# Optimization experiments

Hardware: AMD Instinct MI355X
Metric: run time of the kernel (lower is better)

The kernel has to match this reference:

```python
import math
import jax, jax.numpy as jnp
import numpy as np

B, NQ, NK, DIM, H, HD = 2, 1024, 2048, 1024, 16, 64


def setup_inputs() -> dict:
    key = jax.random.key(0)
    ks = jax.random.split(key, 12)
    s = 1.0 / math.sqrt(DIM)
    return {
        "q": jax.random.normal(ks[0], (B, NQ, DIM), jnp.float32),
        "k": jax.random.normal(ks[1], (B, NK, DIM), jnp.float32),
        "v": jax.random.normal(ks[2], (B, NK, DIM), jnp.float32),
        "distances": jax.random.uniform(ks[3], (B, NQ, NK), jnp.float32),
        "attn_mask": jax.random.bernoulli(ks[4], 0.5, (B, NQ, NK)),
        "key_padding_mask_q": jax.random.bernoulli(ks[5], 0.5, (B, NQ)),
        "key_padding_mask_k": jax.random.bernoulli(ks[6], 0.5, (B, NK)),
        "Wq": jax.random.normal(ks[7], (H * HD, DIM), jnp.float32) * s,
        "Wk": jax.random.normal(ks[8], (H * HD, DIM), jnp.float32) * s,
        "Wv": jax.random.normal(ks[9], (H * HD, DIM), jnp.float32) * s,
        "Wo": jax.random.normal(ks[10], (DIM, H * HD), jnp.float32) * s,
        "gate_alpha": jnp.float32(0.1),
    }


def reference(q, k, v, distances, attn_mask, key_padding_mask_q,
              key_padding_mask_k, Wq, Wk, Wv, Wo, gate_alpha):
    bsz, q_len, _ = q.shape
    k_len = k.shape[1]
    neg = jnp.finfo(q.dtype).min

    # projections -> (B, H, N, HD)
    qp = (q @ Wq.T).reshape(bsz, q_len, H, HD).transpose(0, 2, 1, 3)
    kp = (k @ Wk.T).reshape(bsz, k_len, H, HD).transpose(0, 2, 1, 3)
    vp = (v @ Wv.T).reshape(bsz, k_len, H, HD).transpose(0, 2, 1, 3)

    scores = jnp.einsum('bhqd,bhkd->bhqk', qp, kp) / math.sqrt(HD)
    scores = jnp.where(attn_mask[:, None, :, :], scores, neg)
    scores = jnp.where(key_padding_mask_k[:, None, None, :], scores, neg)

    attn = jax.nn.softmax(scores, axis=-1)  # (B,H,NQ,NK)

    # distance gating: mask, batch-mean normalize, exponential gate
    d = distances * attn_mask.astype(distances.dtype)
    d = d * key_padding_mask_k[:, None, :].astype(d.dtype)
    mean = d.sum(axis=(-1, -2)) / (q_len * k_len + 1e-6)
    mean = jnp.maximum(mean, 1e-6)[:, None, None]
    d = d / mean
    alpha = jax.nn.softplus(gate_alpha)
    gate = jnp.exp(-alpha * d)[:, None, :, :]  # (B,1,NQ,NK)

    w = attn * gate
    w = w / (w.sum(axis=-1, keepdims=True) + 1e-6)

    out = jnp.einsum('bhqk,bhkd->bhqd', w, vp)
    out = out.transpose(0, 2, 1, 3).reshape(bsz, q_len, H * HD)
    out = out * key_padding_mask_q[:, :, None].astype(out.dtype)
    return out @ Wo.T
```

## Files before the change

kernel.cpp:

```cpp
#include <hip/hip_runtime.h>
#include <hip/hip_bf16.h>
#include <cfloat>

#define B_   2
#define NQ_  1024
#define NK_  2048
#define H_   16
#define HD_  64
#define VPAD 2176
#define GPAD 2112

typedef float  floatx4 __attribute__((ext_vector_type(4)));
typedef __bf16 bf16x8  __attribute__((ext_vector_type(8)));
typedef __bf16 bf16x4  __attribute__((ext_vector_type(4)));

static __device__ __forceinline__ floatx4 mfma16(bf16x8 a, bf16x8 b, floatx4 c) {
    return __builtin_amdgcn_mfma_f32_16x16x32_bf16(a, b, c, 0, 0, 0);
}

static __device__ __forceinline__ void gl_lds(const __bf16* g, __bf16* lbase,
                                              int lane) {
#if __has_builtin(__builtin_amdgcn_global_load_lds)
    __builtin_amdgcn_global_load_lds(
        (const __attribute__((address_space(1))) void*)g,
        (__attribute__((address_space(3))) void*)lbase, 16, 0, 0);
#else
    *(bf16x8*)(lbase + lane * 8) = *(const bf16x8*)g;
#endif
}

struct CvtArgs {
    const float* src[7];
    __bf16*      dst[7];
};

__global__ __launch_bounds__(256) void cvt_mean_kernel(
    CvtArgs a, const float* __restrict__ dist, const int* __restrict__ amask,
    const int* __restrict__ kpmk, float* __restrict__ msum,
    __bf16* __restrict__ dmask)
{
    if (blockIdx.x >= 1792) {
        const int mb = blockIdx.x - 1792;
        const int b  = mb >> 9;
        const float* d  = dist  + (size_t)b * NQ_ * NK_;
        const int*   am = amask + (size_t)b * NQ_ * NK_;
        const int*   km = kpmk  + b * NK_;
        __bf16*      dm = dmask + (size_t)b * NQ_ * GPAD;
        const int base = (mb & 511) * 256 + threadIdx.x;
        float s = 0.f;
        #pragma unroll
        for (int j = 0; j < 4; j++) {
            const int i   = base + j * 131072;
            const int idx = i * 4;
            const int kk  = idx & (NK_ - 1);
            const int q   = i >> 9;
            float4 dv = *(const float4*)(d + idx);
            int4   mv = *(const int4*)(am + idx);
            int4   kv = *(const int4*)(km + kk);
            bf16x4 o;
            if (mv.x && kv.x) { s += dv.x; o[0] = (__bf16)dv.x; } else o[0] = (__bf16)3e38f;
            if (mv.y && kv.y) { s += dv.y; o[1] = (__bf16)dv.y; } else o[1] = (__bf16)3e38f;
            if (mv.z && kv.z) { s += dv.z; o[2] = (__bf16)dv.z; } else o[2] = (__bf16)3e38f;
            if (mv.w && kv.w) { s += dv.w; o[3] = (__bf16)dv.w; } else o[3] = (__bf16)3e38f;
            *(bf16x4*)&dm[(size_t)q * GPAD + kk] = o;
        }
        #pragma unroll
        for (int off = 32; off >= 1; off >>= 1) s += __shfl_down(s, off);
        __shared__ float wsum[4];
        if ((threadIdx.x & 63) == 0) wsum[threadIdx.x >> 6] = s;
        __syncthreads();
        if (threadIdx.x == 0)
            atomicAdd(&msum[b], wsum[0] + wsum[1] + wsum[2] + wsum[3]);
        return;
    }
    #pragma unroll
    for (int j = 0; j < 4; j++) {
        size_t r = (size_t)blockIdx.x * 1024 + j * 256 + threadIdx.x;
        int s;
        if (r < 262144)                  { s = 0; }
        else if ((r -= 262144) < 524288) { s = 1; }
        else if ((r -= 524288) < 524288) { s = 2; }
        else { r -= 524288; s = 3 + (int)(r >> 17); r &= 131071; }
        const float* sp = a.src[s] + r * 8;
        float4 f0 = *(const float4*)sp;
        float4 f1 = *(const float4*)(sp + 4);
        bf16x8 o;
        o[0] = (__bf16)f0.x; o[1] = (__bf16)f0.y; o[2] = (__bf16)f0.z; o[3] = (__bf16)f0.w;
        o[4] = (__bf16)f1.x; o[5] = (__bf16)f1.y; o[6] = (__bf16)f1.z; o[7] = (__bf16)f1.w;
        *(bf16x8*)(a.dst[s] + r * 8) = o;
    }
}

template <typename EPI>
static __device__ __forceinline__ void gemm128_core(
    const __bf16* __restrict__ A, const __bf16* __restrict__ Bw,
    int m0, int n0, __bf16* As, __bf16* Bs, EPI epi)
{
    const int t    = threadIdx.x;
    const int w    = t >> 6, lane = t & 63;
    const int lrow = lane & 15, quad = lane >> 4;
    const int lr   = lane >> 2, lc = lane & 3;

    floatx4 acc[4][4];
    #pragma unroll
    for (int mi = 0; mi < 4; mi++)
        #pragma unroll
        for (int ni = 0; ni < 4; ni++) acc[mi][ni] = floatx4{0.f, 0.f, 0.f, 0.f};

    const __bf16* ga = A  + (size_t)(m0 + w * 32 + lr) * 1024 + lc * 8;
    const __bf16* gb = Bw + (size_t)(n0 + w * 32 + lr) * 1024 + lc * 8;

    for (int k0 = 0; k0 < 1024; k0 += 64) {
        __syncthreads();
        #pragma unroll
        for (int h = 0; h < 2; h++) {
            gl_lds(ga + k0 + h * 32,             &As[h * 4096 + (w * 32) * 32],      lane);
            gl_lds(ga + k0 + h * 32 + 16 * 1024, &As[h * 4096 + (w * 32 + 16) * 32], lane);
            gl_lds(gb + k0 + h * 32,             &Bs[h * 4096 + (w * 32) * 32],      lane);
            gl_lds(gb + k0 + h * 32 + 16 * 1024, &Bs[h * 4096 + (w * 32 + 16) * 32], lane);
        }
        __syncthreads();

        #pragma unroll
        for (int h = 0; h < 2; h++) {
            bf16x8 af[4], bfr[4];
            #pragma unroll
            for (int mi = 0; mi < 4; mi++)
                af[mi] = *(const bf16x8*)
                    &As[h * 4096 + ((w & 1) * 64 + mi * 16 + lrow) * 32 + quad * 8];
            #pragma unroll
            for (int ni = 0; ni < 4; ni++)
                bfr[ni] = *(const bf16x8*)
                    &Bs[h * 4096 + ((w >> 1) * 64 + ni * 16 + lrow) * 32 + quad * 8];
            #pragma unroll
            for (int mi = 0; mi < 4; mi++)
                #pragma unroll
                for (int ni = 0; ni < 4; ni++)
                    acc[mi][ni] = mfma16(af[mi], bfr[ni], acc[mi][ni]);
        }
    }

    #pragma unroll
    for (int mi = 0; mi < 4; mi++)
        #pragma unroll
        for (int ni = 0; ni < 4; ni++)
            #pragma unroll
            for (int r = 0; r < 4; r++) {
                const int m = m0 + (w & 1) * 64 + mi * 16 + quad * 4 + r;
                const int n = n0 + (w >> 1) * 64 + ni * 16 + lrow;
                epi(m, n, acc[mi][ni][r]);
            }
}

template <typename EPI>
static __device__ __forceinline__ void gemm64_core(
    const __bf16* __restrict__ A, const __bf16* __restrict__ Bw,
    int m0, int n0, EPI epi)
{
    __shared__ alignas(16) __bf16 As[2][64 * 32];
    __shared__ alignas(16) __bf16 Bs[2][128 * 32];
    const int t    = threadIdx.x;
    const int w    = t >> 6, lane = t & 63;
    const int lrow = lane & 15, quad = lane >> 4;
    const int lr   = lane >> 2, lc = lane & 3;

    floatx4 acc[4][2];
    #pragma unroll
    for (int mi = 0; mi < 4; mi++)
        #pragma unroll
        for (int ni = 0; ni < 2; ni++) acc[mi][ni] = floatx4{0.f, 0.f, 0.f, 0.f};

    const __bf16* ga = A  + (size_t)(m0 + w * 16 + lr) * 1024 + lc * 8;
    const __bf16* gb = Bw + (size_t)(n0 + w * 32 + lr) * 1024 + lc * 8;

    for (int k0 = 0; k0 < 1024; k0 += 64) {
        __syncthreads();
        #pragma unroll
        for (int h = 0; h < 2; h++) {
            gl_lds(ga + k0 + h * 32,             &As[h][(w * 16) * 32],      lane);
            gl_lds(gb + k0 + h * 32,             &Bs[h][(w * 32) * 32],      lane);
            gl_lds(gb + k0 + h * 32 + 16 * 1024, &Bs[h][(w * 32 + 16) * 32], lane);
        }
        __syncthreads();

        #pragma unroll
        for (int h = 0; h < 2; h++) {
            bf16x8 af[4], bfr[2];
            #pragma unroll
            for (int mi = 0; mi < 4; mi++)
                af[mi] = *(const bf16x8*)
                    &As[h][(mi * 16 + lrow) * 32 + quad * 8];
            #pragma unroll
            for (int ni = 0; ni < 2; ni++)
                bfr[ni] = *(const bf16x8*)
                    &Bs[h][(w * 32 + ni * 16 + lrow) * 32 + quad * 8];
            #pragma unroll
            for (int mi = 0; mi < 4; mi++)
                #pragma unroll
                for (int ni = 0; ni < 2; ni++)
                    acc[mi][ni] = mfma16(af[mi], bfr[ni], acc[mi][ni]);
        }
    }

    #pragma unroll
    for (int mi = 0; mi < 4; mi++)
        #pragma unroll
        for (int ni = 0; ni < 2; ni++)
            #pragma unroll
            for (int r = 0; r < 4; r++) {
                const int m = m0 + mi * 16 + quad * 4 + r;
                const int n = n0 + w * 32 + ni * 16 + lrow;
                epi(m, n, acc[mi][ni][r]);
            }
}

__global__ __launch_bounds__(256) void proj_kernel(
    const __bf16* __restrict__ qb, const __bf16* __restrict__ kb,
    const __bf16* __restrict__ vb, const __bf16* __restrict__ wqb,
    const __bf16* __restrict__ wkb, const __bf16* __restrict__ wvb,
    __bf16* __restrict__ qp, __bf16* __restrict__ kp,
    __bf16* __restrict__ vpT)
{
    __shared__ alignas(16) __bf16 As[2 * 128 * 32];
    __shared__ alignas(16) __bf16 Bs[2 * 128 * 32];
    const int z = blockIdx.z;
    if (z == 0) {
        if ((int)blockIdx.x >= 16) return;
        gemm128_core(qb, wqb, blockIdx.x * 128, blockIdx.y * 128, As, Bs,
                     [&](int m, int n, float v) {
            const int b = m >> 10, q = m & 1023;
            const int h = n >> 6,  d = n & 63;
            qp[(((size_t)(b * 16 + h) * NQ_ + q) << 6) + d] = (__bf16)v;
        });
    } else if (z == 1) {
        gemm128_core(kb, wkb, blockIdx.x * 128, blockIdx.y * 128, As, Bs,
                     [&](int m, int n, float v) {
            const int b = m >> 11, key = m & 2047;
            const int h = n >> 6,  d = n & 63;
            kp[(((size_t)(b * 16 + h) * NK_ + key) << 6) + d] = (__bf16)v;
        });
    } else {
        gemm128_core(wvb, vb, blockIdx.y * 128, blockIdx.x * 128, As, Bs,
                     [&](int m, int n, float v) {
            const int h = m >> 6,  d = m & 63;
            const int b = n >> 11, key = n & 2047;
            vpT[((size_t)(b * 16 + h) * HD_ + d) * VPAD + key] = (__bf16)v;
        });
    }
}

__global__ __launch_bounds__(256) void oproj_kernel(
    const __bf16* __restrict__ A, const __bf16* __restrict__ W,
    float* __restrict__ Cout)
{
    const int m0 = blockIdx.x * 64, n0 = blockIdx.y * 128;
    gemm64_core(A, W, m0, n0, [&](int m, int n, float v) {
        Cout[(size_t)m * 1024 + n] = v;
    });
}

__global__ __launch_bounds__(256, 2) void attn_kernel(
    const __bf16* __restrict__ qp, const __bf16* __restrict__ kp,
    const __bf16* __restrict__ vpT, const __bf16* __restrict__ dmask,
    const float* __restrict__ msum, const float* __restrict__ galpha,
    const int* __restrict__ kpmq, __bf16* __restrict__ attnout)
{
    __shared__ __bf16 Ks[64 * 72];
    __shared__ __bf16 Vt[2][64 * 72];
    __shared__ __bf16 Ps[4][2][16 * 72];
    const int t    = threadIdx.x;
    const int w    = t >> 6, lane = t & 63;
    const int lrow = lane & 15, quad = lane >> 4;
    const int qt   = blockIdx.x;
    const int bh   = blockIdx.y;
    const int b    = bh >> 4, h = bh & 15;
    const int q0   = qt * 64 + w * 16;
    const int NT   = NK_ / 64;

    const float mean  = fmaxf(msum[b] / ((float)(NQ_ * NK_) + 1e-6f), 1e-6f);
    const float alpha = log1pf(__expf(galpha[0]));
    const float cg    = -alpha / mean;

    const __bf16* qb = qp + ((size_t)bh * NQ_ + q0 + lrow) * HD_ + quad * 8;
    const bf16x8 qf0 = *(const bf16x8*)qb;
    const bf16x8 qf1 = *(const bf16x8*)(qb + 32);

    const int srow0 = t >> 3,        sc0 = t & 7;
    const int srow1 = 32 + (t >> 3), sc1 = t & 7;
    const int so0 = srow0 * 72 + sc0 * 8;
    const int so1 = srow1 * 72 + sc1 * 8;
    const __bf16* Kg = kp  + (size_t)bh * NK_ * HD_;
    const __bf16* Vg = vpT + (size_t)bh * HD_ * VPAD;
    const __bf16* grow = dmask + ((size_t)b * NQ_ + q0 + lrow) * GPAD;

    float G = 0.f;
    floatx4 O[4];
    #pragma unroll
    for (int nb = 0; nb < 4; nb++) O[nb] = floatx4{0.f, 0.f, 0.f, 0.f};

    bf16x8 kr0, kr1, vr0, vr1;
    bf16x4 gr[4];
    auto loadt = [&](int kb) {
        kr0 = *(const bf16x8*)(Kg + (size_t)(kb + srow0) * HD_ + sc0 * 8);
        kr1 = *(const bf16x8*)(Kg + (size_t)(kb + srow1) * HD_ + sc1 * 8);
        vr0 = *(const bf16x8*)(Vg + (size_t)srow0 * VPAD + kb + sc0 * 8);
        vr1 = *(const bf16x8*)(Vg + (size_t)srow1 * VPAD + kb + sc1 * 8);
        #pragma unroll
        for (int c = 0; c < 4; c++)
            gr[c] = *(const bf16x4*)(grow + kb + c * 16 + quad * 4);
    };
    loadt(0);

    for (int ib = 0; ib < NT; ib++) {
        const int kb  = ib * 64;
        const int cur = ib & 1;

        __syncthreads();
        *(bf16x8*)&Ks[so0]      = kr0;
        *(bf16x8*)&Ks[so1]      = kr1;
        *(bf16x8*)&Vt[cur][so0] = vr0;
        *(bf16x8*)&Vt[cur][so1] = vr1;
        __syncthreads();

        bf16x4 gcur[4];
        #pragma unroll
        for (int c = 0; c < 4; c++) gcur[c] = gr[c];
        if (ib + 1 < NT) loadt(kb + 64);

        floatx4 s4[4];
        #pragma unroll
        for (int c = 0; c < 4; c++) {
            bf16x8 kf0 = *(const bf16x8*)&Ks[(c * 16 + lrow) * 72 + quad * 8];
            bf16x8 kf1 = *(const bf16x8*)&Ks[(c * 16 + lrow) * 72 + 32 + quad * 8];
            floatx4 a = floatx4{0.f, 0.f, 0.f, 0.f};
            a = mfma16(kf0, qf0, a);
            a = mfma16(kf1, qf1, a);
            s4[c] = a;
        }

        if (ib > 0) {
            const int prv = cur ^ 1;
            bf16x8 pf0 = *(const bf16x8*)&Ps[w][prv][lrow * 72 + quad * 8];
            bf16x8 pf1 = *(const bf16x8*)&Ps[w][prv][lrow * 72 + 32 + quad * 8];
            #pragma unroll
            for (int nb = 0; nb < 4; nb++) {
                bf16x8 vf0 = *(const bf16x8*)
                    &Vt[prv][(nb * 16 + lrow) * 72 + quad * 8];
                bf16x8 vf1 = *(const bf16x8*)
                    &Vt[prv][(nb * 16 + lrow) * 72 + 32 + quad * 8];
                O[nb] = mfma16(pf0, vf0, O[nb]);
                O[nb] = mfma16(pf1, vf1, O[nb]);
            }
        }

        #pragma unroll
        for (int c = 0; c < 4; c++) {
            const float e0 = __expf(fmaf(s4[c][0], 0.125f, cg * (float)gcur[c][0]));
            const float e1 = __expf(fmaf(s4[c][1], 0.125f, cg * (float)gcur[c][1]));
            const float e2 = __expf(fmaf(s4[c][2], 0.125f, cg * (float)gcur[c][2]));
            const float e3 = __expf(fmaf(s4[c][3], 0.125f, cg * (float)gcur[c][3]));
            G += (e0 + e1) + (e2 + e3);
            bf16x4 pk;
            pk[0] = (__bf16)e0; pk[1] = (__bf16)e1;
            pk[2] = (__bf16)e2; pk[3] = (__bf16)e3;
            *(bf16x4*)&Ps[w][cur][lrow * 72 + c * 16 + quad * 4] = pk;
        }
    }

    {
        const int prv = (NT - 1) & 1;
        bf16x8 pf0 = *(const bf16x8*)&Ps[w][prv][lrow * 72 + quad * 8];
        bf16x8 pf1 = *(const bf16x8*)&Ps[w][prv][lrow * 72 + 32 + quad * 8];
        #pragma unroll
        for (int nb = 0; nb < 4; nb++) {
            bf16x8 vf0 = *(const bf16x8*)&Vt[prv][(nb * 16 + lrow) * 72 + quad * 8];
            bf16x8 vf1 = *(const bf16x8*)&Vt[prv][(nb * 16 + lrow) * 72 + 32 + quad * 8];
            O[nb] = mfma16(pf0, vf0, O[nb]);
            O[nb] = mfma16(pf1, vf1, O[nb]);
        }
    }

    G += __shfl_xor(G, 16);
    G += __shfl_xor(G, 32);

    #pragma unroll
    for (int r = 0; r < 4; r++) {
        const int q  = q0 + quad * 4 + r;
        const float gq = __shfl(G, quad * 4 + r);
        const float f  = kpmq[b * NQ_ + q] ? 1.f / (gq + 1e-30f) : 0.f;
        #pragma unroll
        for (int nb = 0; nb < 4; nb++) {
            attnout[((size_t)b * NQ_ + q) * 1024 + h * HD_ + nb * 16 + lrow] =
                (__bf16)(O[nb][r] * f);
        }
    }
}

extern "C" void kernel_launch(void* const* d_in, const int* in_sizes, int n_in,
                              void* d_out, int out_size, void* d_ws,
                              size_t ws_size, hipStream_t stream)
{
    const float* q      = (const float*)d_in[0];
    const float* k      = (const float*)d_in[1];
    const float* v      = (const float*)d_in[2];
    const float* dist   = (const float*)d_in[3];
    const int*   amask  = (const int*)d_in[4];
    const int*   kpmq   = (const int*)d_in[5];
    const int*   kpmk   = (const int*)d_in[6];
    const float* Wq     = (const float*)d_in[7];
    const float* Wk     = (const float*)d_in[8];
    const float* Wv     = (const float*)d_in[9];
    const float* Wo     = (const float*)d_in[10];
    const float* galpha = (const float*)d_in[11];

    char* p = (char*)d_ws;
    float*  msum = (float*)p;                 p += 256;
    __bf16* qb   = (__bf16*)p;                p += (size_t)2097152 * 2;
    __bf16* kb   = (__bf16*)p;                p += (size_t)4194304 * 2;
    __bf16* vb   = (__bf16*)p;                p += (size_t)4194304 * 2;
    __bf16* wqb  = (__bf16*)p;                p += (size_t)1048576 * 2;
    __bf16* wkb  = (__bf16*)p;                p += (size_t)1048576 * 2;
    __bf16* wvb  = (__bf16*)p;                p += (size_t)1048576 * 2;
    __bf16* wob  = (__bf16*)p;                p += (size_t)1048576 * 2;
    __bf16* qp   = (__bf16*)p;                p += (size_t)2097152 * 2;
    __bf16* kpb  = (__bf16*)p;                p += (size_t)4194304 * 2;
    __bf16* vpT  = (__bf16*)p;                p += (size_t)32 * 64 * VPAD * 2;
    __bf16* dmask = (__bf16*)p;               p += (size_t)2048 * GPAD * 2;
    __bf16* attnout = (__bf16*)p;             p += (size_t)2097152 * 2;

    CvtArgs ca;
    ca.src[0] = q;  ca.src[1] = k;  ca.src[2] = v;
    ca.src[3] = Wq; ca.src[4] = Wk; ca.src[5] = Wv; ca.src[6] = Wo;
    ca.dst[0] = qb;  ca.dst[1] = kb;  ca.dst[2] = vb;
    ca.dst[3] = wqb; ca.dst[4] = wkb; ca.dst[5] = wvb; ca.dst[6] = wob;

    hipMemsetAsync(msum, 0, 256, stream);
    cvt_mean_kernel<<<2816, 256, 0, stream>>>(ca, dist, amask, kpmk, msum,
                                              dmask);
    proj_kernel<<<dim3(32, 8, 3), 256, 0, stream>>>(qb, kb, vb, wqb, wkb, wvb,
                                                    qp, kpb, vpT);
    attn_kernel<<<dim3(16, 32), 256, 0, stream>>>(qp, kpb, vpT, dmask,
                                                  msum, galpha, kpmq, attnout);
    oproj_kernel<<<dim3(32, 8), 256, 0, stream>>>(attnout, wob, (float*)d_out);
}
```

Baseline: 245.6 us.

## Split key range across two wave groups per block and merge partials in LDS

The attention kernel now runs 512 threads per block, with two groups of four waves each processing half of the key sequence for the same query tile. Partial output accumulators and row sums from the second group are written to shared memory and added by the first group before normalization. This doubles the number of waves in flight and halves each wave's serial loop. In exchange it drops the one-tile-delayed PV pipelining, adds LDS usage and a final merge step with extra barriers.

Measured after the change: 248.2 us. About the same (+1.0%).

```diff
diff --git a/kernel.cpp b/kernel.cpp
--- a/kernel.cpp
+++ b/kernel.cpp
@@ -259,23 +259,28 @@
     });
 }
 
-__global__ __launch_bounds__(256, 2) void attn_kernel(
+__global__ __launch_bounds__(512, 4) void attn_kernel(
     const __bf16* __restrict__ qp, const __bf16* __restrict__ kp,
     const __bf16* __restrict__ vpT, const __bf16* __restrict__ dmask,
     const float* __restrict__ msum, const float* __restrict__ galpha,
     const int* __restrict__ kpmq, __bf16* __restrict__ attnout)
 {
-    __shared__ __bf16 Ks[64 * 72];
+    __shared__ __bf16 Ks[2][64 * 72];
     __shared__ __bf16 Vt[2][64 * 72];
-    __shared__ __bf16 Ps[4][2][16 * 72];
+    __shared__ __bf16 Ps[8][16 * 72];
+    __shared__ float  Ox[4][16][68];
+    __shared__ float  Gx[4][16];
     const int t    = threadIdx.x;
     const int w    = t >> 6, lane = t & 63;
+    const int g    = w >> 2;
+    const int wg   = w & 3;
     const int lrow = lane & 15, quad = lane >> 4;
     const int qt   = blockIdx.x;
     const int bh   = blockIdx.y;
     const int b    = bh >> 4, h = bh & 15;
-    const int q0   = qt * 64 + w * 16;
-    const int NT   = NK_ / 64;
+    const int q0   = qt * 64 + wg * 16;
+    const int k0   = g * (NK_ / 2);
+    const int NT   = (NK_ / 2) / 64;
 
     const float mean  = fmaxf(msum[b] / ((float)(NQ_ * NK_) + 1e-6f), 1e-6f);
     const float alpha = log1pf(__expf(galpha[0]));
@@ -285,8 +290,9 @@
     const bf16x8 qf0 = *(const bf16x8*)qb;
     const bf16x8 qf1 = *(const bf16x8*)(qb + 32);
 
-    const int srow0 = t >> 3,        sc0 = t & 7;
-    const int srow1 = 32 + (t >> 3), sc1 = t & 7;
+    const int tg    = t & 255;
+    const int srow0 = tg >> 3,        sc0 = tg & 7;
+    const int srow1 = 32 + (tg >> 3), sc1 = tg & 7;
     const int so0 = srow0 * 72 + sc0 * 8;
     const int so1 = srow1 * 72 + sc1 * 8;
     const __bf16* Kg = kp  + (size_t)bh * NK_ * HD_;
@@ -309,17 +315,16 @@
         for (int c = 0; c < 4; c++)
             gr[c] = *(const bf16x4*)(grow + kb + c * 16 + quad * 4);
     };
-    loadt(0);
+    loadt(k0);
 
     for (int ib = 0; ib < NT; ib++) {
-        const int kb  = ib * 64;
-        const int cur = ib & 1;
-
-        __syncthreads();
-        *(bf16x8*)&Ks[so0]      = kr0;
-        *(bf16x8*)&Ks[so1]      = kr1;
-        *(bf16x8*)&Vt[cur][so0] = vr0;
-        *(bf16x8*)&Vt[cur][so1] = vr1;
+        const int kb = k0 + ib * 64;
+
+        __syncthreads();
+        *(bf16x8*)&Ks[g][so0] = kr0;
+        *(bf16x8*)&Ks[g][so1] = kr1;
+        *(bf16x8*)&Vt[g][so0] = vr0;
+        *(bf16x8*)&Vt[g][so1] = vr1;
         __syncthreads();
 
         bf16x4 gcur[4];
@@ -330,27 +335,12 @@
         floatx4 s4[4];
         #pragma unroll
         for (int c = 0; c < 4; c++) {
-            bf16x8 kf0 = *(const bf16x8*)&Ks[(c * 16 + lrow) * 72 + quad * 8];
-            bf16x8 kf1 = *(const bf16x8*)&Ks[(c * 16 + lrow) * 72 + 32 + quad * 8];
+            bf16x8 kf0 = *(const bf16x8*)&Ks[g][(c * 16 + lrow) * 72 + quad * 8];
+            bf16x8 kf1 = *(const bf16x8*)&Ks[g][(c * 16 + lrow) * 72 + 32 + quad * 8];
             floatx4 a = floatx4{0.f, 0.f, 0.f, 0.f};
             a = mfma16(kf0, qf0, a);
             a = mfma16(kf1, qf1, a);
             s4[c] = a;
-        }
-
-        if (ib > 0) {
-            const int prv = cur ^ 1;
-            bf16x8 pf0 = *(const bf16x8*)&Ps[w][prv][lrow * 72 + quad * 8];
-            bf16x8 pf1 = *(const bf16x8*)&Ps[w][prv][lrow * 72 + 32 + quad * 8];
-            #pragma unroll
-            for (int nb = 0; nb < 4; nb++) {
-                bf16x8 vf0 = *(const bf16x8*)
-                    &Vt[prv][(nb * 16 + lrow) * 72 + quad * 8];
-                bf16x8 vf1 = *(const bf16x8*)
-                    &Vt[prv][(nb * 16 + lrow) * 72 + 32 + quad * 8];
-                O[nb] = mfma16(pf0, vf0, O[nb]);
-                O[nb] = mfma16(pf1, vf1, O[nb]);
-            }
         }
 
         #pragma unroll
@@ -363,35 +353,50 @@
             bf16x4 pk;
             pk[0] = (__bf16)e0; pk[1] = (__bf16)e1;
             pk[2] = (__bf16)e2; pk[3] = (__bf16)e3;
-            *(bf16x4*)&Ps[w][cur][lrow * 72 + c * 16 + quad * 4] = pk;
-        }
-    }
-
-    {
-        const int prv = (NT - 1) & 1;
-        bf16x8 pf0 = *(const bf16x8*)&Ps[w][prv][lrow * 72 + quad * 8];
-        bf16x8 pf1 = *(const bf16x8*)&Ps[w][prv][lrow * 72 + 32 + quad * 8];
-        #pragma unroll
-        for (int nb = 0; nb < 4; nb++) {
-            bf16x8 vf0 = *(const bf16x8*)&Vt[prv][(nb * 16 + lrow) * 72 + quad * 8];
-            bf16x8 vf1 = *(const bf16x8*)&Vt[prv][(nb * 16 + lrow) * 72 + 32 + quad * 8];
-            O[nb] = mfma16(pf0, vf0, O[nb]);
-            O[nb] = mfma16(pf1, vf1, O[nb]);
+            *(bf16x4*)&Ps[w][lrow * 72 + c * 16 + quad * 4] = pk;
+        }
+
+        {
+            bf16x8 pf0 = *(const bf16x8*)&Ps[w][lrow * 72 + quad * 8];
+            bf16x8 pf1 = *(const bf16x8*)&Ps[w][lrow * 72 + 32 + quad * 8];
+            #pragma unroll
+            for (int nb = 0; nb < 4; nb++) {
+                bf16x8 vf0 = *(const bf16x8*)
+                    &Vt[g][(nb * 16 + lrow) * 72 + quad * 8];
+                bf16x8 vf1 = *(const bf16x8*)
+                    &Vt[g][(nb * 16 + lrow) * 72 + 32 + quad * 8];
+                O[nb] = mfma16(pf0, vf0, O[nb]);
+                O[nb] = mfma16(pf1, vf1, O[nb]);
+            }
         }
     }
 
     G += __shfl_xor(G, 16);
     G += __shfl_xor(G, 32);
 
-    #pragma unroll
-    for (int r = 0; r < 4; r++) {
-        const int q  = q0 + quad * 4 + r;
-        const float gq = __shfl(G, quad * 4 + r);
-        const float f  = kpmq[b * NQ_ + q] ? 1.f / (gq + 1e-30f) : 0.f;
-        #pragma unroll
-        for (int nb = 0; nb < 4; nb++) {
-            attnout[((size_t)b * NQ_ + q) * 1024 + h * HD_ + nb * 16 + lrow] =
-                (__bf16)(O[nb][r] * f);
+    __syncthreads();
+    if (g == 1) {
+        #pragma unroll
+        for (int nb = 0; nb < 4; nb++)
+            #pragma unroll
+            for (int r = 0; r < 4; r++)
+                Ox[wg][quad * 4 + r][nb * 16 + lrow] = O[nb][r];
+        if (quad == 0) Gx[wg][lrow] = G;
+    }
+    __syncthreads();
+    if (g == 0) {
+        #pragma unroll
+        for (int r = 0; r < 4; r++) {
+            const int j  = quad * 4 + r;
+            const int q  = q0 + j;
+            const float gq = __shfl(G, j) + Gx[wg][j];
+            const float f  = kpmq[b * NQ_ + q] ? 1.f / (gq + 1e-30f) : 0.f;
+            #pragma unroll
+            for (int nb = 0; nb < 4; nb++) {
+                const float ov = O[nb][r] + Ox[wg][j][nb * 16 + lrow];
+                attnout[((size_t)b * NQ_ + q) * 1024 + h * HD_ + nb * 16 + lrow] =
+                    (__bf16)(ov * f);
+            }
         }
     }
 }
@@ -439,7 +444,7 @@
                                               dmask);
     proj_kernel<<<dim3(32, 8, 3), 256, 0, stream>>>(qb, kb, vb, wqb, wkb, wvb,
                                                     qp, kpb, vpT);
-    attn_kernel<<<dim3(16, 32), 256, 0, stream>>>(qp, kpb, vpT, dmask,
+    attn_kernel<<<dim3(16, 32), 512, 0, stream>>>(qp, kpb, vpT, dmask,
                                                   msum, galpha, kpmq, attnout);
     oproj_kernel<<<dim3(32, 8), 256, 0, stream>>>(attnout, wob, (float*)d_out);
 }
```
